# Kernel tuning notes

Measured on AMD Instinct MI355X. Metric: run time of the kernel, lower is better.

## Reference

```python
import jax, jax.numpy as jnp
import numpy as np

B, S_LEN, H, NH, NT, NL, I = 8, 2048, 768, 12, 32, 9, 3072
SPAN = 64
NSP = S_LEN // SPAN
TAG_RATE = 2
DH = H // NH
EPS = 1e-12


def rope(x):
    # interleaved-pair rotary position embedding, x: [B, L, H]
    L = x.shape[1]
    half = x.shape[2] // 2
    inv = 1.0 / (10000.0 ** (jnp.arange(half, dtype=jnp.float32) / half))
    ang = jnp.arange(L, dtype=jnp.float32)[:, None] * inv[None, :]  # [L, half]
    sin, cos = jnp.sin(ang), jnp.cos(ang)
    x2 = x.reshape(x.shape[0], L, half, 2)
    xe, xo = x2[..., 0], x2[..., 1]
    return jnp.stack([xe * cos - xo * sin, xe * sin + xo * cos], axis=-1).reshape(x.shape)


def layernorm(x, g, b):
    m = jnp.mean(x, axis=-1, keepdims=True)
    v = jnp.mean((x - m) ** 2, axis=-1, keepdims=True)
    return (x - m) * jax.lax.rsqrt(v + EPS) * g + b


def mha(q_in, kv_in, Wqkv, bqkv, Wo, bo):
    # torch nn.MultiheadAttention math (eval), batched over leading span axis
    Wq, Wk, Wv = jnp.split(Wqkv, 3, axis=0)
    bq, bk, bv = jnp.split(bqkv, 3)
    def heads(x, W, b):
        return (x @ W.T + b).reshape(x.shape[0], x.shape[1], NH, DH)
    q = heads(q_in, Wq, bq)
    k = heads(kv_in, Wk, bk)
    v = heads(kv_in, Wv, bv)
    scores = jnp.einsum('nqhd,nkhd->nhqk', q, k) * (1.0 / DH ** 0.5)
    a = jax.nn.softmax(scores, axis=-1)
    o = jnp.einsum('nhqk,nkhd->nqhd', a, v).reshape(q_in.shape[0], q_in.shape[1], H)
    return o @ Wo.T + bo


def setup_inputs() -> dict:
    key = jax.random.key(0)
    ks = jax.random.split(key, 16)
    p = lambda i, shape: (0.02 * jax.random.normal(ks[i], shape)).astype(jnp.float32)
    inp = {}
    inp['word_embedding'] = jax.random.normal(ks[0], (B, S_LEN, H), dtype=jnp.float32)
    # fixed-length, non-overlapping spans covering the sequence
    inp['span_starts'] = jnp.broadcast_to(jnp.arange(NSP, dtype=jnp.int32) * SPAN, (B, NSP))
    inp['span_tags'] = jax.random.randint(ks[1], (B, NSP), 0, NT)
    inp['tag_emb'] = p(2, (NT, H))
    inp['sa_Wqkv'] = p(3, (3 * H, H)); inp['sa_bqkv'] = jnp.zeros((3 * H,), jnp.float32)
    inp['sa_Wo'] = p(4, (H, H)); inp['sa_bo'] = jnp.zeros((H,), jnp.float32)
    inp['at_Wqkv'] = p(5, (3 * H, H)); inp['at_bqkv'] = jnp.zeros((3 * H,), jnp.float32)
    inp['at_Wo'] = p(6, (H, H)); inp['at_bo'] = jnp.zeros((H,), jnp.float32)
    inp['an_g'] = jnp.ones((H,), jnp.float32); inp['an_b'] = jnp.zeros((H,), jnp.float32)
    inp['W1'] = p(7, (I, H)); inp['b1'] = jnp.zeros((I,), jnp.float32)
    inp['W2'] = p(8, (H, I)); inp['b2'] = jnp.zeros((H,), jnp.float32)
    inp['fn_g'] = jnp.ones((H,), jnp.float32); inp['fn_b'] = jnp.zeros((H,), jnp.float32)
    inp['Wout'] = p(9, (NL, H)); inp['bout'] = jnp.zeros((NL,), jnp.float32)
    return inp


def reference(word_embedding, span_starts, span_tags, tag_emb,
              sa_Wqkv, sa_bqkv, sa_Wo, sa_bo,
              at_Wqkv, at_bqkv, at_Wo, at_bo,
              an_g, an_b, W1, b1, W2, b2, fn_g, fn_b, Wout, bout):
    raw = word_embedding  # hidden dropout p=0 (eval) -> identity
    xe = rope(word_embedding)
    # pack all spans: [B, NSP*SPAN] token positions
    pos = (span_starts[..., None] + jnp.arange(SPAN)).reshape(B, NSP * SPAN)
    spans = jnp.take_along_axis(xe, pos[..., None], axis=1).reshape(B * NSP, SPAN, H)
    # if_add_a_self_attention: X += self_attention(X, X, X)
    X = spans + mha(spans, spans, sa_Wqkv, sa_bqkv, sa_Wo, sa_bo)
    # enumerate_mode == 'self_attention': prepend tag embedding token, self-attend, drop it
    tagv = tag_emb[span_tags.reshape(-1)][:, None, :]  # [B*NSP, 1, H]
    qkv = jnp.concatenate([tagv, X], axis=1)           # [B*NSP, SPAN+1, H]
    res = mha(qkv, qkv, at_Wqkv, at_bqkv, at_Wo, at_bo)[:, 1:, :]
    # scatter-add results back into the full sequence
    taged = jnp.zeros_like(word_embedding).at[jnp.arange(B)[:, None], pos].add(
        res.reshape(B, NSP * SPAN, H))
    # if_merge_by_add branch
    out_emb = layernorm(raw + taged * TAG_RATE, an_g, an_b)
    ff = jax.nn.relu(out_emb @ W1.T + b1) @ W2.T + b2
    out = layernorm(ff + out_emb, fn_g, fn_b)
    return out @ Wout.T + bout
```

## Files before the change

kernel.cpp:

```cpp
#include <hip/hip_runtime.h>


typedef __attribute__((ext_vector_type(8))) short short8;
typedef __attribute__((ext_vector_type(4))) float f32x4;

typedef const __attribute__((address_space(1))) unsigned int* gas1_t;
typedef __attribute__((address_space(3))) unsigned int* las3_t;

#define DEVI static __device__ __forceinline__

DEVI void gload_lds16(const void* g, void* l){
  __builtin_amdgcn_global_load_lds((gas1_t)g, (las3_t)l, 16, 0, 0);
}

template<int N> DEVI void vmcnt_imm(){
  if constexpr (N == 8) asm volatile("s_waitcnt vmcnt(8)" ::: "memory");
  else if constexpr (N == 4) asm volatile("s_waitcnt vmcnt(4)" ::: "memory");
  else asm volatile("s_waitcnt vmcnt(0)" ::: "memory");
}

DEVI unsigned short f2bf(float f){
  union { float f; unsigned u; } v; v.f = f;
  unsigned u = v.u;
  return (unsigned short)((u + 0x7fffu + ((u >> 16) & 1u)) >> 16);
}
DEVI float bf2f(unsigned short h){
  union { unsigned u; float f; } v; v.u = ((unsigned)h) << 16; return v.f;
}

__global__ void k_ropetab(float2* __restrict__ tab){
  int idx = blockIdx.x * 256 + threadIdx.x;
  if (idx >= 2048 * 384) return;
  int l = idx / 384, i = idx % 384;
  float inv = __expf(-(float)i * (9.210340371976184f / 384.0f));
  float ang = (float)l * inv;
  tab[idx] = make_float2(cosf(ang), sinf(ang));
}

__global__ void k_f2bf_all(const float* __restrict__ s0, const float* __restrict__ s1,
                           const float* __restrict__ s2, const float* __restrict__ s3,
                           const float* __restrict__ s4, const float* __restrict__ s5,
                           unsigned short* __restrict__ dst){
  int i = blockIdx.x * 256 + threadIdx.x;
  int e = i * 4;
  const float* src; int off;
  if      (e < 1769472){ src = s0; off = e; }
  else if (e < 2359296){ src = s1; off = e - 1769472; }
  else if (e < 4128768){ src = s2; off = e - 2359296; }
  else if (e < 4718592){ src = s3; off = e - 4128768; }
  else if (e < 7077888){ src = s4; off = e - 4718592; }
  else                 { src = s5; off = e - 7077888; }
  float4 v = *(const float4*)(src + off);
  ushort4 o;
  o.x = f2bf(v.x); o.y = f2bf(v.y); o.z = f2bf(v.z); o.w = f2bf(v.w);
  *(ushort4*)(dst + e) = o;
}

__global__ void k_gather_rope(const float* __restrict__ we, const int* __restrict__ starts,
                              const float2* __restrict__ tab, unsigned short* __restrict__ spans){
  int idx = blockIdx.x * 256 + threadIdx.x;
  int r  = idx / 192;
  int c4 = idx % 192;
  int span = r >> 6, s = r & 63;
  int b = span >> 5;
  int l = starts[span] + s;
  float4 x = *(const float4*)(we + ((size_t)b * 2048 + l) * 768 + c4 * 4);
  int i0 = c4 * 2;
  float2 cs0 = tab[l * 384 + i0];
  float2 cs1 = tab[l * 384 + i0 + 1];
  ushort4 o;
  o.x = f2bf(x.x * cs0.x - x.y * cs0.y);
  o.y = f2bf(x.x * cs0.y + x.y * cs0.x);
  o.z = f2bf(x.z * cs1.x - x.w * cs1.y);
  o.w = f2bf(x.z * cs1.y + x.w * cs1.x);
  *(ushort4*)(spans + (size_t)r * 768 + c4 * 4) = o;
}

__global__ void k_fill_tag(const float* __restrict__ tag_emb, const int* __restrict__ tags,
                           unsigned short* __restrict__ at_in){
  int span = blockIdx.x;
  int tag = tags[span];
  const float* src = tag_emb + (size_t)tag * 768;
  unsigned short* dst = at_in + (size_t)span * 65 * 768;
  for (int j = threadIdx.x; j < 768; j += 256) dst[j] = f2bf(src[j]);
}

template<int EPI, int SPLIT>
__global__ __launch_bounds__(512, 2)
void k_gemm256(const unsigned short* __restrict__ A, const unsigned short* __restrict__ Bw,
               const float* __restrict__ bias, void* __restrict__ outp,
               unsigned short* __restrict__ resid, int M, int N, int K, int nbx)
{
  __shared__ unsigned short Asl[4 * 256 * 32];
  __shared__ unsigned short Bsl[4 * 256 * 32];
  const int t0 = threadIdx.x;
  const int w = t0 >> 6, lane = t0 & 63;
  const int g = lane >> 4, li = lane & 15;
  const int wm = w >> 2, wn = w & 3;

  int nwg = gridDim.x;
  int bid = blockIdx.x;
  int koff = 0, Keff = K;
  bool sl = false;
  if (SPLIT){
    const int halfg = nwg >> 1;
    sl = bid >= halfg;
    if (sl) bid -= halfg;
    nwg = halfg;
    Keff = K >> 1;
    koff = sl ? Keff : 0;
  }

  const int q = nwg >> 3, r8 = nwg & 7;
  const int xcd = bid & 7, off = bid >> 3;
  const int swz = (xcd < r8 ? xcd * (q + 1) : r8 * (q + 1) + (xcd - r8) * q) + off;
  int mt, nt;
  const int main_ = nbx << 6;
  if (swz >= main_){ mt = 64; nt = swz - main_; }
  else {
    const int s = swz / 12, wv = swz % 12;
    const int nsc = nbx / 3;
    mt = (s / nsc) * 4 + (wv & 3);
    nt = (s % nsc) * 3 + (wv >> 2);
  }
  const int m0 = mt * 256, n0 = nt * 256;

  const int srow = lane >> 2;
  const int sgc = (((lane & 3) ^ ((lane >> 3) & 3)) << 3);
  const int cs = ((g ^ ((li >> 1) & 3)) << 3);

  f32x4 acc[8][4];
  #pragma unroll
  for (int i = 0; i < 8; i++)
    #pragma unroll
    for (int j = 0; j < 4; j++) acc[i][j] = f32x4{0.f, 0.f, 0.f, 0.f};

  const int KT = Keff >> 5;

  #define STAGE(t_, s_) do { \
    const unsigned short* ga0 = A  + (size_t)(m0 +       w*16 + srow) * K + koff + (t_)*32 + sgc; \
    const unsigned short* ga1 = A  + (size_t)(m0 + 128 + w*16 + srow) * K + koff + (t_)*32 + sgc; \
    const unsigned short* gb0 = Bw + (size_t)(n0 +       w*16 + srow) * K + koff + (t_)*32 + sgc; \
    const unsigned short* gb1 = Bw + (size_t)(n0 + 128 + w*16 + srow) * K + koff + (t_)*32 + sgc; \
    gload_lds16(ga0, Asl + (s_)*8192 + (      w*16)*32); \
    gload_lds16(ga1, Asl + (s_)*8192 + (128 + w*16)*32); \
    gload_lds16(gb0, Bsl + (s_)*8192 + (      w*16)*32); \
    gload_lds16(gb1, Bsl + (s_)*8192 + (128 + w*16)*32); \
  } while(0)

  STAGE(0, 0);
  STAGE(1, 1);
  STAGE(2, 2);
  vmcnt_imm<8>();
  __builtin_amdgcn_s_barrier();

  for (int t = 0; t < KT; ++t){
    const int slot = t & 3;
    const unsigned short* As = Asl + slot * 8192;
    const unsigned short* Bs = Bsl + slot * 8192;

    short8 af[8], bfr[4];
    #pragma unroll
    for (int m = 0; m < 8; m++)
      af[m] = *(const short8*)(As + (wm * 128 + m * 16 + li) * 32 + cs);
    #pragma unroll
    for (int n = 0; n < 4; n++)
      bfr[n] = *(const short8*)(Bs + (wn * 64 + n * 16 + li) * 32 + cs);

    if (t + 3 < KT) STAGE(t + 3, (t + 3) & 3);

    __builtin_amdgcn_s_setprio(1);
    #pragma unroll
    for (int m = 0; m < 8; m++)
      #pragma unroll
      for (int n = 0; n < 4; n++)
        acc[m][n] = __builtin_amdgcn_mfma_f32_16x16x32_bf16(af[m], bfr[n], acc[m][n], 0, 0, 0);
    __builtin_amdgcn_s_setprio(0);

    if (t + 1 < KT){
      __builtin_amdgcn_sched_barrier(0);
      if (t + 3 < KT)      vmcnt_imm<8>();
      else if (t + 2 < KT) vmcnt_imm<4>();
      else                 vmcnt_imm<0>();
      __builtin_amdgcn_s_barrier();
    }
  }
  #undef STAGE

  unsigned short* outb = SPLIT ? (sl ? resid : (unsigned short*)outp)
                               : (unsigned short*)outp;
  float* outf = (float*)outp;
  #pragma unroll
  for (int m = 0; m < 8; m++){
    const int row = m0 + wm * 128 + m * 16 + g * 4;
    #pragma unroll
    for (int n = 0; n < 4; n++){
      const int col = n0 + wn * 64 + n * 16 + li;
      const float bv = (SPLIT && sl) ? 0.f : bias[col];
      #pragma unroll
      for (int r = 0; r < 4; r++){
        float v = acc[m][n][r] + bv;
        const int orow = row + r;
        if (EPI == 1) v += bf2f(resid[(size_t)orow * N + col]);
        if (EPI == 3) v = v > 0.f ? v : 0.f;
        if (EPI == 2 && !SPLIT){
          outf[(size_t)orow * N + col] = v;
        } else if (EPI == 1){
          outb[(size_t)(orow + orow / 64 + 1) * N + col] = f2bf(v);
        } else {
          outb[(size_t)orow * N + col] = f2bf(v);
        }
      }
    }
  }
}

template<int AT>
__global__ __launch_bounds__(64)
void k_attn(const unsigned short* __restrict__ qkv, unsigned short* __restrict__ outp)
{
  constexpr int Lkv  = AT ? 65 : 64;
  constexpr int qoff = AT ? 1 : 0;
  constexpr int NKF  = AT ? 5 : 4;
  constexpr int VK   = AT ? 65 : 64;
  const int h = blockIdx.x;
  const int span = blockIdx.y;
  const int base = span * Lkv;
  const int lane = threadIdx.x;
  const int g = lane >> 4, li = lane & 15;

  __shared__ unsigned short P[64 * 104];
  __shared__ unsigned short Vl[65 * 72 + 8];

  {
    const int vrow = lane >> 4;
    const int vcol = (lane & 15) * 4;
    #pragma unroll
    for (int k0 = 0; k0 < 64; k0 += 4){
      ushort4 v = *(const ushort4*)(qkv + (size_t)(base + k0 + vrow) * 2304 + 1536 + h * 64 + vcol);
      *(ushort4*)(Vl + (k0 + vrow) * 72 + vcol) = v;
    }
    if (AT) Vl[64 * 72 + lane] = qkv[(size_t)(base + 64) * 2304 + 1536 + h * 64 + lane];
  }

  short8 qf[4][2];
  #pragma unroll
  for (int m = 0; m < 4; m++)
    #pragma unroll
    for (int kq = 0; kq < 2; kq++)
      qf[m][kq] = *(const short8*)(qkv + (size_t)(base + qoff + m * 16 + li) * 2304 + h * 64 + kq * 32 + g * 8);

  f32x4 sc[4][NKF];
  #pragma unroll
  for (int m = 0; m < 4; m++)
    #pragma unroll
    for (int n = 0; n < NKF; n++) sc[m][n] = f32x4{0.f, 0.f, 0.f, 0.f};

  #pragma unroll
  for (int kq = 0; kq < 2; kq++){
    #pragma unroll
    for (int n = 0; n < NKF; n++){
      int krow = n * 16 + li; if (krow >= Lkv) krow = Lkv - 1;
      short8 kf = *(const short8*)(qkv + (size_t)(base + krow) * 2304 + 768 + h * 64 + kq * 32 + g * 8);
      #pragma unroll
      for (int m = 0; m < 4; m++)
        sc[m][n] = __builtin_amdgcn_mfma_f32_16x16x32_bf16(qf[m][kq], kf, sc[m][n], 0, 0, 0);
    }
  }

  const float scale = 0.125f;
  #pragma unroll
  for (int m = 0; m < 4; m++){
    #pragma unroll
    for (int r = 0; r < 4; r++){
      float mx = -1e30f;
      #pragma unroll
      for (int n = 0; n < NKF; n++){
        float v = sc[m][n][r] * scale;
        if (n * 16 + li >= VK) v = -1e30f;
        sc[m][n][r] = v;
        mx = fmaxf(mx, v);
      }
      mx = fmaxf(mx, __shfl_xor(mx, 1, 64));
      mx = fmaxf(mx, __shfl_xor(mx, 2, 64));
      mx = fmaxf(mx, __shfl_xor(mx, 4, 64));
      mx = fmaxf(mx, __shfl_xor(mx, 8, 64));
      float sum = 0.f;
      #pragma unroll
      for (int n = 0; n < NKF; n++){
        float p = __expf(sc[m][n][r] - mx);
        sc[m][n][r] = p;
        sum += p;
      }
      sum += __shfl_xor(sum, 1, 64);
      sum += __shfl_xor(sum, 2, 64);
      sum += __shfl_xor(sum, 4, 64);
      sum += __shfl_xor(sum, 8, 64);
      const float inv = 1.f / sum;
      const int prow = m * 16 + g * 4 + r;
      #pragma unroll
      for (int n = 0; n < NKF; n++)
        P[prow * 104 + n * 16 + li] = f2bf(sc[m][n][r] * inv);
    }
  }
  __syncthreads();

  f32x4 oacc[4][4];
  #pragma unroll
  for (int m = 0; m < 4; m++)
    #pragma unroll
    for (int n = 0; n < 4; n++) oacc[m][n] = f32x4{0.f, 0.f, 0.f, 0.f};

  #pragma unroll
  for (int kp = 0; kp < 2; kp++){
    short8 pf[4];
    #pragma unroll
    for (int m = 0; m < 4; m++)
      pf[m] = *(const short8*)(P + (m * 16 + li) * 104 + kp * 32 + g * 8);
    #pragma unroll
    for (int n = 0; n < 4; n++){
      short8 vf;
      #pragma unroll
      for (int i = 0; i < 8; i++)
        vf[i] = (short)Vl[(kp * 32 + g * 8 + i) * 72 + n * 16 + li];
      #pragma unroll
      for (int m = 0; m < 4; m++)
        oacc[m][n] = __builtin_amdgcn_mfma_f32_16x16x32_bf16(pf[m], vf, oacc[m][n], 0, 0, 0);
    }
  }

  if (AT){
    float v64[4];
    #pragma unroll
    for (int n = 0; n < 4; n++) v64[n] = bf2f(Vl[64 * 72 + n * 16 + li]);
    #pragma unroll
    for (int m = 0; m < 4; m++)
      #pragma unroll
      for (int r = 0; r < 4; r++){
        float p = bf2f(P[(m * 16 + g * 4 + r) * 104 + 64]);
        #pragma unroll
        for (int n = 0; n < 4; n++) oacc[m][n][r] += p * v64[n];
      }
  }

  #pragma unroll
  for (int m = 0; m < 4; m++)
    #pragma unroll
    for (int n = 0; n < 4; n++)
      #pragma unroll
      for (int r = 0; r < 4; r++){
        int q = m * 16 + g * 4 + r;
        outp[(size_t)(span * 64 + q) * 768 + h * 64 + n * 16 + li] = f2bf(oacc[m][n][r]);
      }
}

__global__ __launch_bounds__(256)
void k_ln1(const float* __restrict__ raw, const unsigned short* __restrict__ resa,
           const unsigned short* __restrict__ resb,
           const int* __restrict__ starts, const float* __restrict__ gg,
           const float* __restrict__ bb, unsigned short* __restrict__ oe16)
{
  int wave = threadIdx.x >> 6, lane = threadIdx.x & 63;
  int r = blockIdx.x * 4 + wave;
  int span = r >> 6, s = r & 63;
  int b = span >> 5;
  int l = starts[span] + s;
  const float* rp = raw + ((size_t)b * 2048 + l) * 768;
  const unsigned short* qa = resa + (size_t)r * 768;
  const unsigned short* qb = resb + (size_t)r * 768;
  float x[12];
  float sum = 0.f;
  #pragma unroll
  for (int j = 0; j < 12; j++){
    int c = lane + j * 64;
    x[j] = rp[c] + 2.f * (bf2f(qa[c]) + bf2f(qb[c]));
    sum += x[j];
  }
  #pragma unroll
  for (int o = 1; o < 64; o <<= 1) sum += __shfl_xor(sum, o, 64);
  float mean = sum * (1.f / 768.f);
  float vs = 0.f;
  #pragma unroll
  for (int j = 0; j < 12; j++){ float d = x[j] - mean; vs += d * d; }
  #pragma unroll
  for (int o = 1; o < 64; o <<= 1) vs += __shfl_xor(vs, o, 64);
  float rstd = rsqrtf(vs * (1.f / 768.f) + 1e-12f);
  size_t ob = ((size_t)b * 2048 + l) * 768;
  #pragma unroll
  for (int j = 0; j < 12; j++){
    int c = lane + j * 64;
    float y = (x[j] - mean) * rstd * gg[c] + bb[c];
    oe16[ob + c] = f2bf(y);
  }
}

__global__ __launch_bounds__(256)
void k_ln2_out(const unsigned short* __restrict__ ff2, const unsigned short* __restrict__ oe,
               const float* __restrict__ gg, const float* __restrict__ bb,
               const float* __restrict__ Wout, const float* __restrict__ bout,
               float* __restrict__ out)
{
  int wave = threadIdx.x >> 6, lane = threadIdx.x & 63;
  int t = blockIdx.x * 4 + wave;
  const unsigned short* fp = ff2 + (size_t)t * 768;
  const unsigned short* ep = oe  + (size_t)t * 768;
  float x[12];
  float sum = 0.f;
  #pragma unroll
  for (int j = 0; j < 12; j++){
    int c = lane + j * 64;
    x[j] = bf2f(fp[c]) + bf2f(ep[c]);
    sum += x[j];
  }
  #pragma unroll
  for (int o = 1; o < 64; o <<= 1) sum += __shfl_xor(sum, o, 64);
  float mean = sum * (1.f / 768.f);
  float vs = 0.f;
  #pragma unroll
  for (int j = 0; j < 12; j++){ float d = x[j] - mean; vs += d * d; }
  #pragma unroll
  for (int o = 1; o < 64; o <<= 1) vs += __shfl_xor(vs, o, 64);
  float rstd = rsqrtf(vs * (1.f / 768.f) + 1e-12f);
  #pragma unroll
  for (int j = 0; j < 12; j++){
    int c = lane + j * 64;
    x[j] = (x[j] - mean) * rstd * gg[c] + bb[c];
  }
  for (int n = 0; n < 9; n++){
    float p = 0.f;
    #pragma unroll
    for (int j = 0; j < 12; j++){
      int c = lane + j * 64;
      p += x[j] * Wout[n * 768 + c];
    }
    #pragma unroll
    for (int o = 1; o < 64; o <<= 1) p += __shfl_xor(p, o, 64);
    if (lane == 0) out[(size_t)t * 9 + n] = p + bout[n];
  }
}

extern "C" void kernel_launch(void* const* d_in, const int* in_sizes, int n_in,
                              void* d_out, int out_size, void* d_ws, size_t ws_size,
                              hipStream_t stream)
{
  const float* we      = (const float*)d_in[0];
  const int*   starts  = (const int*)d_in[1];
  const int*   tags    = (const int*)d_in[2];
  const float* tag_emb = (const float*)d_in[3];
  const float* sa_Wqkv = (const float*)d_in[4];
  const float* sa_bqkv = (const float*)d_in[5];
  const float* sa_Wo   = (const float*)d_in[6];
  const float* sa_bo   = (const float*)d_in[7];
  const float* at_Wqkv = (const float*)d_in[8];
  const float* at_bqkv = (const float*)d_in[9];
  const float* at_Wo   = (const float*)d_in[10];
  const float* at_bo   = (const float*)d_in[11];
  const float* an_g    = (const float*)d_in[12];
  const float* an_b    = (const float*)d_in[13];
  const float* W1      = (const float*)d_in[14];
  const float* b1      = (const float*)d_in[15];
  const float* W2      = (const float*)d_in[16];
  const float* b2      = (const float*)d_in[17];
  const float* fn_g    = (const float*)d_in[18];
  const float* fn_b    = (const float*)d_in[19];
  const float* Wout    = (const float*)d_in[20];
  const float* bout    = (const float*)d_in[21];
  float* out = (float*)d_out;
  char* ws = (char*)d_ws;

  unsigned short* spans   = (unsigned short*)(ws + 0);
  unsigned short* at_in   = (unsigned short*)(ws + 25165824);
  unsigned short* attno   = (unsigned short*)(ws + 50724864);
  unsigned short* qkv     = (unsigned short*)(ws + 75890688);
  float2*         ropetab = (float2*)(ws + 75890688);
  unsigned short* resa    = (unsigned short*)(ws + 75890688);
  unsigned short* resb    = (unsigned short*)(ws + 101056512);
  unsigned short* oe16    = (unsigned short*)(ws + 0);
  unsigned short* ff1     = (unsigned short*)(ws + 25165824);
  unsigned short* ff2     = (unsigned short*)(ws + 125829120);
  unsigned short* wb      = (unsigned short*)(ws + 152567808);
  unsigned short* sa_Wqkv_b = wb;
  unsigned short* sa_Wo_b   = sa_Wqkv_b + 2304 * 768;
  unsigned short* at_Wqkv_b = sa_Wo_b   + 768 * 768;
  unsigned short* at_Wo_b   = at_Wqkv_b + 2304 * 768;
  unsigned short* W1_b      = at_Wo_b   + 768 * 768;
  unsigned short* W2_b      = W1_b      + 3072 * 768;

  k_ropetab<<<3072, 256, 0, stream>>>(ropetab);
  k_f2bf_all<<<9216, 256, 0, stream>>>(sa_Wqkv, sa_Wo, at_Wqkv, at_Wo, W1, W2, wb);
  k_gather_rope<<<12288, 256, 0, stream>>>(we, starts, ropetab, spans);

  k_gemm256<0,0><<<576, 512, 0, stream>>>(spans, sa_Wqkv_b, sa_bqkv, qkv, nullptr, 16384, 2304, 768, 9);
  k_attn<0><<<dim3(12, 256), 64, 0, stream>>>(qkv, attno);
  k_fill_tag<<<256, 256, 0, stream>>>(tag_emb, tags, at_in);
  k_gemm256<1,0><<<192, 512, 0, stream>>>(attno, sa_Wo_b, sa_bo, at_in, spans, 16384, 768, 768, 3);
  k_gemm256<0,0><<<585, 512, 0, stream>>>(at_in, at_Wqkv_b, at_bqkv, qkv, nullptr, 16640, 2304, 768, 9);
  k_attn<1><<<dim3(12, 256), 64, 0, stream>>>(qkv, attno);
  k_gemm256<0,1><<<384, 512, 0, stream>>>(attno, at_Wo_b, at_bo, resa, resb, 16384, 768, 768, 3);
  k_ln1<<<4096, 256, 0, stream>>>(we, resa, resb, starts, an_g, an_b, oe16);
  k_gemm256<3,0><<<768, 512, 0, stream>>>(oe16, W1_b, b1, ff1, nullptr, 16384, 3072, 768, 12);
  k_gemm256<0,0><<<192, 512, 0, stream>>>(ff1, W2_b, b2, ff2, nullptr, 16384, 768, 3072, 3);
  k_ln2_out<<<4096, 256, 0, stream>>>(ff2, oe16, fn_g, fn_b, Wout, bout, out);
}
```

Measured before the change: 503.9 us.

## Switch GEMM to BK=64 double-buffered LDS pipeline with 8-way swizzle

Restructures the 256x256 GEMM main loop from a 4-stage pipeline with K-tiles of 32 to a 2-stage pipeline with K-tiles of 64. LDS use stays the same. Each iteration runs two MFMA sub-steps and there are half as many barriers and waits. The XOR swizzle is widened to 8 chunks to fit the 64-wide rows. The trade-off is a shallower prefetch: only one tile is in flight and the loop waits for vmcnt(0) every iteration, which may expose global-load latency.

```diff
diff --git a/kernel.cpp b/kernel.cpp
--- a/kernel.cpp
+++ b/kernel.cpp
@@ -91,8 +91,8 @@
                const float* __restrict__ bias, void* __restrict__ outp,
                unsigned short* __restrict__ resid, int M, int N, int K, int nbx)
 {
-  __shared__ unsigned short Asl[4 * 256 * 32];
-  __shared__ unsigned short Bsl[4 * 256 * 32];
+  __shared__ unsigned short Asl[2 * 256 * 64];
+  __shared__ unsigned short Bsl[2 * 256 * 64];
   const int t0 = threadIdx.x;
   const int w = t0 >> 6, lane = t0 & 63;
   const int g = lane >> 4, li = lane & 15;
@@ -125,9 +125,10 @@
   }
   const int m0 = mt * 256, n0 = nt * 256;
 
-  const int srow = lane >> 2;
-  const int sgc = (((lane & 3) ^ ((lane >> 3) & 3)) << 3);
-  const int cs = ((g ^ ((li >> 1) & 3)) << 3);
+  const int srow = lane >> 3;
+  const int sgc = (((lane & 7) ^ (lane >> 3)) << 3);
+  const int cs0 = ((g       ^ (li & 7)) << 3);
+  const int cs1 = (((g + 4) ^ (li & 7)) << 3);
 
   f32x4 acc[8][4];
   #pragma unroll
@@ -135,39 +136,45 @@
     #pragma unroll
     for (int j = 0; j < 4; j++) acc[i][j] = f32x4{0.f, 0.f, 0.f, 0.f};
 
-  const int KT = Keff >> 5;
-
-  #define STAGE(t_, s_) do { \
-    const unsigned short* ga0 = A  + (size_t)(m0 +       w*16 + srow) * K + koff + (t_)*32 + sgc; \
-    const unsigned short* ga1 = A  + (size_t)(m0 + 128 + w*16 + srow) * K + koff + (t_)*32 + sgc; \
-    const unsigned short* gb0 = Bw + (size_t)(n0 +       w*16 + srow) * K + koff + (t_)*32 + sgc; \
-    const unsigned short* gb1 = Bw + (size_t)(n0 + 128 + w*16 + srow) * K + koff + (t_)*32 + sgc; \
-    gload_lds16(ga0, Asl + (s_)*8192 + (      w*16)*32); \
-    gload_lds16(ga1, Asl + (s_)*8192 + (128 + w*16)*32); \
-    gload_lds16(gb0, Bsl + (s_)*8192 + (      w*16)*32); \
-    gload_lds16(gb1, Bsl + (s_)*8192 + (128 + w*16)*32); \
+  const int KT = Keff >> 6;
+
+  #define STAGE_A64(t_, s_) do { \
+    _Pragma("unroll") \
+    for (int j = 0; j < 4; j++){ \
+      const unsigned short* ga = A + (size_t)(m0 + w*32 + j*8 + srow) * K + koff + (t_)*64 + sgc; \
+      gload_lds16(ga, Asl + (s_)*16384 + (w*32 + j*8)*64); \
+    } \
   } while(0)
-
-  STAGE(0, 0);
-  STAGE(1, 1);
-  STAGE(2, 2);
-  vmcnt_imm<8>();
+  #define STAGE_B64(t_, s_) do { \
+    _Pragma("unroll") \
+    for (int j = 0; j < 4; j++){ \
+      const unsigned short* gb = Bw + (size_t)(n0 + w*32 + j*8 + srow) * K + koff + (t_)*64 + sgc; \
+      gload_lds16(gb, Bsl + (s_)*16384 + (w*32 + j*8)*64); \
+    } \
+  } while(0)
+
+  STAGE_A64(0, 0);
+  STAGE_B64(0, 0);
+  vmcnt_imm<0>();
   __builtin_amdgcn_s_barrier();
 
   for (int t = 0; t < KT; ++t){
-    const int slot = t & 3;
-    const unsigned short* As = Asl + slot * 8192;
-    const unsigned short* Bs = Bsl + slot * 8192;
+    const int slot = t & 1;
+    const unsigned short* As = Asl + slot * 16384;
+    const unsigned short* Bs = Bsl + slot * 16384;
 
     short8 af[8], bfr[4];
     #pragma unroll
     for (int m = 0; m < 8; m++)
-      af[m] = *(const short8*)(As + (wm * 128 + m * 16 + li) * 32 + cs);
+      af[m] = *(const short8*)(As + (wm * 128 + m * 16 + li) * 64 + cs0);
     #pragma unroll
     for (int n = 0; n < 4; n++)
-      bfr[n] = *(const short8*)(Bs + (wn * 64 + n * 16 + li) * 32 + cs);
-
-    if (t + 3 < KT) STAGE(t + 3, (t + 3) & 3);
+      bfr[n] = *(const short8*)(Bs + (wn * 64 + n * 16 + li) * 64 + cs0);
+
+    if (t + 1 < KT){
+      STAGE_A64(t + 1, slot ^ 1);
+      STAGE_B64(t + 1, slot ^ 1);
+    }
 
     __builtin_amdgcn_s_setprio(1);
     #pragma unroll
@@ -177,15 +184,29 @@
         acc[m][n] = __builtin_amdgcn_mfma_f32_16x16x32_bf16(af[m], bfr[n], acc[m][n], 0, 0, 0);
     __builtin_amdgcn_s_setprio(0);
 
+    #pragma unroll
+    for (int m = 0; m < 8; m++)
+      af[m] = *(const short8*)(As + (wm * 128 + m * 16 + li) * 64 + cs1);
+    #pragma unroll
+    for (int n = 0; n < 4; n++)
+      bfr[n] = *(const short8*)(Bs + (wn * 64 + n * 16 + li) * 64 + cs1);
+
+    __builtin_amdgcn_s_setprio(1);
+    #pragma unroll
+    for (int m = 0; m < 8; m++)
+      #pragma unroll
+      for (int n = 0; n < 4; n++)
+        acc[m][n] = __builtin_amdgcn_mfma_f32_16x16x32_bf16(af[m], bfr[n], acc[m][n], 0, 0, 0);
+    __builtin_amdgcn_s_setprio(0);
+
     if (t + 1 < KT){
       __builtin_amdgcn_sched_barrier(0);
-      if (t + 3 < KT)      vmcnt_imm<8>();
-      else if (t + 2 < KT) vmcnt_imm<4>();
-      else                 vmcnt_imm<0>();
+      vmcnt_imm<0>();
       __builtin_amdgcn_s_barrier();
     }
   }
-  #undef STAGE
+  #undef STAGE_A64
+  #undef STAGE_B64
 
   unsigned short* outb = SPLIT ? (sl ? resid : (unsigned short*)outp)
                                : (unsigned short*)outp;
```

Measured after the change: 488.0 us. -3.1%, faster.
